# Optimization experiments

Measured on AMD Instinct MI355X. Metric: run time of the kernel, lower is better.

## Reference

```python
import jax, jax.numpy as jnp
import numpy as np

B = 512          # batch
SIZE_IN = 1024   # input features
SIZE_OUT = 256   # output features
NUM_Q = 16       # quantiles


def setup_inputs() -> dict:
    key = jax.random.key(0)
    k1, k2, k3, k4 = jax.random.split(key, 4)
    x = jax.random.normal(k1, (B, SIZE_IN), dtype=jnp.float32)
    indices = jax.random.randint(k2, (B, SIZE_IN), 0, NUM_Q, dtype=jnp.int64)
    # param_index table: row (q*SIZE_IN + j) holds a SIZE_OUT weight vector
    param_table = jax.random.normal(k3, (NUM_Q * SIZE_IN, SIZE_OUT), dtype=jnp.float32)
    bias = jax.random.normal(k4, (SIZE_OUT,), dtype=jnp.float32)
    return {"x": x, "indices": indices, "param_table": param_table, "bias": bias}


def reference(x, indices, param_table, bias):
    size_in = x.shape[1]
    # flat row index into the quantile-indexed table: q*size_in + feature_pos
    flat_idx = indices * size_in + jnp.arange(size_in, dtype=indices.dtype)[None, :]  # [B, In]
    gathered = param_table[flat_idx]  # [B, In, Out] gather
    # scale each gathered weight vector by the scalar input and reduce over features
    out = jnp.einsum('bi,bio->bo', x, gathered)  # [B, Out]
    return out + bias
```

## Files before the change

### kernel.cpp

```cpp
#include <hip/hip_runtime.h>
#include <stdint.h>


constexpr int SIZE_IN  = 1024;
constexpr int SIZE_OUT = 256;
constexpr int TM = 32;
constexpr int TN = 128;
constexpr int A_STRIDE = 1032;

typedef short short8   __attribute__((ext_vector_type(8)));
typedef float floatx4  __attribute__((ext_vector_type(4)));

__device__ inline uint32_t pack2bf(float lo, float hi) {
    uint32_t a = __float_as_uint(lo) + 0x8000u;
    uint32_t b = __float_as_uint(hi) + 0x8000u;
    return __builtin_amdgcn_perm(b, a, 0x07060302);
}

__global__ __launch_bounds__(256, 2)
void idxlin_mfma(const float* __restrict__ x,
                 const int*   __restrict__ idx,
                 const float* __restrict__ table,
                 const float* __restrict__ bias,
                 float*       __restrict__ out)
{
    __shared__ uint16_t Alds[TM * A_STRIDE];

    const int tid = threadIdx.x;
    const int q   = blockIdx.x & 15;
    const int r   = blockIdx.x >> 4;
    const int nh  = r & 1;
    const int bt  = r >> 1;
    const int b0  = bt * TM;
    const int n0  = nh * TN;

    const float4* x4 = reinterpret_cast<const float4*>(x   + b0 * SIZE_IN);
    const int4*   i4 = reinterpret_cast<const int4*>(idx + b0 * SIZE_IN);
    #pragma unroll 4
    for (int s = 0; s < TM; ++s) {
        const int f = s * 256 + tid;
        const float4 xv = x4[f];
        const int4   iv = i4[f];
        const float v0 = (iv.x == q) ? xv.x : 0.f;
        const float v1 = (iv.y == q) ? xv.y : 0.f;
        const float v2 = (iv.z == q) ? xv.z : 0.f;
        const float v3 = (iv.w == q) ? xv.w : 0.f;
        uint2 d;
        d.x = pack2bf(v0, v1);
        d.y = pack2bf(v2, v3);
        *reinterpret_cast<uint2*>(&Alds[s * A_STRIDE + tid * 4]) = d;
    }
    __syncthreads();

    const int lane  = tid & 63;
    const int w     = tid >> 6;
    const int nlane = lane & 15;
    const int quad  = lane >> 4;

    const float* bp = table + (q * SIZE_IN + quad * 8) * SIZE_OUT + n0 + w * 32 + nlane;
    const uint16_t* arow0 = &Alds[(0 * 16 + nlane) * A_STRIDE + quad * 8];
    const uint16_t* arow1 = &Alds[(1 * 16 + nlane) * A_STRIDE + quad * 8];

    floatx4 acc[2][2] = {{{0.f,0.f,0.f,0.f},{0.f,0.f,0.f,0.f}},
                         {{0.f,0.f,0.f,0.f},{0.f,0.f,0.f,0.f}}};

    #pragma unroll 2
    for (int kb = 0; kb < SIZE_IN / 32; ++kb) {
        float wv[2][8];
        #pragma unroll
        for (int nt = 0; nt < 2; ++nt)
            #pragma unroll
            for (int j = 0; j < 8; ++j)
                wv[nt][j] = bp[j * SIZE_OUT + nt * 16];

        const short8 a0 = *reinterpret_cast<const short8*>(arow0 + kb * 32);
        const short8 a1 = *reinterpret_cast<const short8*>(arow1 + kb * 32);

        #pragma unroll
        for (int nt = 0; nt < 2; ++nt) {
            union { uint32_t u[4]; short8 s; } bf;
            bf.u[0] = pack2bf(wv[nt][0], wv[nt][1]);
            bf.u[1] = pack2bf(wv[nt][2], wv[nt][3]);
            bf.u[2] = pack2bf(wv[nt][4], wv[nt][5]);
            bf.u[3] = pack2bf(wv[nt][6], wv[nt][7]);
            acc[0][nt] = __builtin_amdgcn_mfma_f32_16x16x32_bf16(a0, bf.s, acc[0][nt], 0, 0, 0);
            acc[1][nt] = __builtin_amdgcn_mfma_f32_16x16x32_bf16(a1, bf.s, acc[1][nt], 0, 0, 0);
        }
        bp += 32 * SIZE_OUT;
    }

    #pragma unroll
    for (int mt = 0; mt < 2; ++mt)
        #pragma unroll
        for (int nt = 0; nt < 2; ++nt)
            #pragma unroll
            for (int rr = 0; rr < 4; ++rr) {
                const int bg = b0 + mt * 16 + quad * 4 + rr;
                const int o  = n0 + w * 32 + nt * 16 + nlane;
                atomicAdd(&out[bg * SIZE_OUT + o], acc[mt][nt][rr]);
            }

    if (q == 0) {
        const int o_l = tid & (TN - 1);
        const int m0  = (tid >> 7) * 16;
        const float bv = bias[n0 + o_l];
        #pragma unroll
        for (int rr = 0; rr < 16; ++rr)
            atomicAdd(&out[(b0 + m0 + rr) * SIZE_OUT + n0 + o_l], bv);
    }
}

extern "C" void kernel_launch(void* const* d_in, const int* in_sizes, int n_in,
                              void* d_out, int out_size, void* d_ws, size_t ws_size,
                              hipStream_t stream) {
    const float* x     = (const float*)d_in[0];
    const int*   idx   = (const int*)d_in[1];
    const float* table = (const float*)d_in[2];
    const float* bias  = (const float*)d_in[3];
    float*       out   = (float*)d_out;

    hipMemsetAsync(out, 0, (size_t)out_size * sizeof(float), stream);
    idxlin_mfma<<<dim3(512), dim3(256), 0, stream>>>(x, idx, table, bias, out);
}
```

Baseline: 91.41 us.

## Replace atomic accumulation with per-quantile workspace partials and a reduction kernel

Each block now writes its per-quantile partial output tile to a workspace slice instead of doing atomicAdd into the output. A second kernel sums the 16 quantile slices and adds the bias, which also drops the memset. This removes atomic contention and the memset, at the cost of an extra kernel launch and 8 MB of workspace traffic. If the workspace is too small, the old atomic path is used.

```diff
diff --git a/kernel.cpp b/kernel.cpp
--- a/kernel.cpp
+++ b/kernel.cpp
@@ -4,9 +4,12 @@
 
 constexpr int SIZE_IN  = 1024;
 constexpr int SIZE_OUT = 256;
+constexpr int BATCH    = 512;
 constexpr int TM = 32;
 constexpr int TN = 128;
 constexpr int A_STRIDE = 1032;
+
+constexpr size_t WS_NEED = (size_t)16 * BATCH * SIZE_OUT * sizeof(float);
 
 typedef short short8   __attribute__((ext_vector_type(8)));
 typedef float floatx4  __attribute__((ext_vector_type(4)));
@@ -17,12 +20,14 @@
     return __builtin_amdgcn_perm(b, a, 0x07060302);
 }
 
+template <bool USE_WS>
 __global__ __launch_bounds__(256, 2)
 void idxlin_mfma(const float* __restrict__ x,
                  const int*   __restrict__ idx,
                  const float* __restrict__ table,
                  const float* __restrict__ bias,
-                 float*       __restrict__ out)
+                 float*       __restrict__ out,
+                 float*       __restrict__ ws)
 {
     __shared__ uint16_t Alds[TM * A_STRIDE];
 
@@ -89,25 +94,54 @@
         bp += 32 * SIZE_OUT;
     }
 
+    if (USE_WS) {
+        float* wsq = ws + ((size_t)(q * BATCH + b0)) * SIZE_OUT + n0;
+        #pragma unroll
+        for (int mt = 0; mt < 2; ++mt)
+            #pragma unroll
+            for (int nt = 0; nt < 2; ++nt)
+                #pragma unroll
+                for (int rr = 0; rr < 4; ++rr) {
+                    const int row = mt * 16 + quad * 4 + rr;
+                    const int col = w * 32 + nt * 16 + nlane;
+                    wsq[row * SIZE_OUT + col] = acc[mt][nt][rr];
+                }
+    } else {
+        #pragma unroll
+        for (int mt = 0; mt < 2; ++mt)
+            #pragma unroll
+            for (int nt = 0; nt < 2; ++nt)
+                #pragma unroll
+                for (int rr = 0; rr < 4; ++rr) {
+                    const int bg = b0 + mt * 16 + quad * 4 + rr;
+                    const int o  = n0 + w * 32 + nt * 16 + nlane;
+                    atomicAdd(&out[bg * SIZE_OUT + o], acc[mt][nt][rr]);
+                }
+        if (q == 0) {
+            const int o_l = tid & (TN - 1);
+            const int m0  = (tid >> 7) * 16;
+            const float bv = bias[n0 + o_l];
+            #pragma unroll
+            for (int rr = 0; rr < 16; ++rr)
+                atomicAdd(&out[(b0 + m0 + rr) * SIZE_OUT + n0 + o_l], bv);
+        }
+    }
+}
+
+__global__ __launch_bounds__(256)
+void reduce_ws(const float* __restrict__ ws, const float* __restrict__ bias,
+               float* __restrict__ out)
+{
+    const int e  = blockIdx.x * 256 + threadIdx.x;
+    const int o4 = e & 63;
+    const float4* w4 = reinterpret_cast<const float4*>(ws);
+    float4 s = reinterpret_cast<const float4*>(bias)[o4];
     #pragma unroll
-    for (int mt = 0; mt < 2; ++mt)
-        #pragma unroll
-        for (int nt = 0; nt < 2; ++nt)
-            #pragma unroll
-            for (int rr = 0; rr < 4; ++rr) {
-                const int bg = b0 + mt * 16 + quad * 4 + rr;
-                const int o  = n0 + w * 32 + nt * 16 + nlane;
-                atomicAdd(&out[bg * SIZE_OUT + o], acc[mt][nt][rr]);
-            }
-
-    if (q == 0) {
-        const int o_l = tid & (TN - 1);
-        const int m0  = (tid >> 7) * 16;
-        const float bv = bias[n0 + o_l];
-        #pragma unroll
-        for (int rr = 0; rr < 16; ++rr)
-            atomicAdd(&out[(b0 + m0 + rr) * SIZE_OUT + n0 + o_l], bv);
+    for (int q = 0; q < 16; ++q) {
+        const float4 v = w4[(size_t)q * (BATCH * SIZE_OUT / 4) + e];
+        s.x += v.x; s.y += v.y; s.z += v.z; s.w += v.w;
     }
+    reinterpret_cast<float4*>(out)[e] = s;
 }
 
 extern "C" void kernel_launch(void* const* d_in, const int* in_sizes, int n_in,
@@ -118,7 +152,13 @@
     const float* table = (const float*)d_in[2];
     const float* bias  = (const float*)d_in[3];
     float*       out   = (float*)d_out;
+    float*       ws    = (float*)d_ws;
 
-    hipMemsetAsync(out, 0, (size_t)out_size * sizeof(float), stream);
-    idxlin_mfma<<<dim3(512), dim3(256), 0, stream>>>(x, idx, table, bias, out);
+    if (ws_size >= WS_NEED) {
+        idxlin_mfma<true><<<dim3(512), dim3(256), 0, stream>>>(x, idx, table, bias, out, ws);
+        reduce_ws<<<dim3(BATCH * SIZE_OUT / 4 / 256), dim3(256), 0, stream>>>(ws, bias, out);
+    } else {
+        hipMemsetAsync(out, 0, (size_t)out_size * sizeof(float), stream);
+        idxlin_mfma<false><<<dim3(512), dim3(256), 0, stream>>>(x, idx, table, bias, out, ws);
+    }
 }
```

Result: faster. 89.60 us (-2.0%).
